# Kernel optimization log

Hardware: AMD Instinct MI355X
Metric: run time of the kernel (lower is better)

Reference implementation:

```python
import jax, jax.numpy as jnp
import numpy as np
import math

B, T, E = 2, 2048, 1024
D = 1024          # total inner dim (config.head_dim)
H = 16            # n_head
HD = D // H       # per-head dim = 64


def setup_inputs() -> dict:
    key = jax.random.key(0)
    k1, k2, k3, k4, k5 = jax.random.split(key, 5)
    s = 0.02
    return {
        "x": jax.random.normal(k1, (B, T, E), dtype=jnp.float32),
        "W_attn": jax.random.normal(k2, (E, 3 * D), dtype=jnp.float32) * s,
        "b_attn": jnp.zeros((3 * D,), dtype=jnp.float32),
        "W_proj": jax.random.normal(k3, (D, E), dtype=jnp.float32) * s,
        "b_proj": jnp.zeros((E,), dtype=jnp.float32),
    }


def reference(x, W_attn, b_attn, W_proj, b_proj):
    Bc, Tc, _ = x.shape
    qkv = x @ W_attn + b_attn                       # [B,T,3D]
    q, k, v = jnp.split(qkv, 3, axis=-1)            # each [B,T,D]
    # reshape to heads: [B,H,T,hd]
    q = q.reshape(Bc, Tc, H, HD).transpose(0, 2, 1, 3)
    k = k.reshape(Bc, Tc, H, HD).transpose(0, 2, 1, 3)
    v = v.reshape(Bc, Tc, H, HD).transpose(0, 2, 1, 3)
    scale = 1.0 / math.sqrt(HD)
    att = jnp.einsum("bhqd,bhkd->bhqk", q, k) * scale   # [B,H,T,T]
    causal = jnp.tril(jnp.ones((Tc, Tc), dtype=bool))
    att = jnp.where(causal[None, None], att, -jnp.inf)
    att = jax.nn.softmax(att, axis=-1)
    y = jnp.einsum("bhqk,bhkd->bhqd", att, v)           # [B,H,T,hd]
    y = y.transpose(0, 2, 1, 3).reshape(Bc, Tc, D)      # [B,T,D]
    return y @ W_proj + b_proj                          # [B,T,E]
```

## Files before the change

kernel.cpp:

```cpp
#include <hip/hip_runtime.h>

typedef unsigned short u16;
typedef unsigned char u8;
typedef signed char s8;
typedef unsigned int u32;
typedef short bf16x8 __attribute__((ext_vector_type(8)));
typedef float f32x4 __attribute__((ext_vector_type(4)));
typedef int i32x4 __attribute__((ext_vector_type(4)));

#define SXI 21.1666667f
#define SWI 1058.3333f
#define DEQ 4.4640015e-5f

__device__ __forceinline__ u16 f2bf(float f) {
  union { float f; u32 u; } v; v.f = f;
  u32 r = v.u + 0x7fffu + ((v.u >> 16) & 1u);
  return (u16)(r >> 16);
}
__device__ __forceinline__ u16 f2bf_fast(float f) {
  union { float f; u32 u; } v; v.f = f;
  return (u16)((v.u + 0x8000u) >> 16);
}
__device__ __forceinline__ s8 q8(float v, float s) {
  float x = fminf(127.f, fmaxf(-127.f, v * s));
  return (s8)__float2int_rn(x);
}
__device__ __forceinline__ float fexp2(float x) {
#if __has_builtin(__builtin_amdgcn_exp2f)
  return __builtin_amdgcn_exp2f(x);
#else
  return exp2f(x);
#endif
}

__device__ __forceinline__ void gld_lds16(const u16* g, u16* l) {
  __builtin_amdgcn_global_load_lds(
      (__attribute__((address_space(1))) u32*)(g),
      (__attribute__((address_space(3))) u32*)(l), 16, 0, 0);
}
__device__ __forceinline__ void gld_lds16b(const u8* g, u8* l) {
  __builtin_amdgcn_global_load_lds(
      (__attribute__((address_space(1))) u32*)(g),
      (__attribute__((address_space(3))) u32*)(l), 16, 0, 0);
}

__device__ __forceinline__ bf16x8 ldsfrag(const u16* base, int row, int c8) {
  return *(const bf16x8*)(base + row * 64 + ((c8 ^ (row & 7)) << 3));
}
__device__ __forceinline__ int swz4(int r) { return (r & 3) ^ ((r >> 2) & 3); }

template <int CTRL>
__device__ __forceinline__ float dppf(float x) {
  return __int_as_float(__builtin_amdgcn_update_dpp(0, __float_as_int(x), CTRL, 0xf, 0xf, true));
}
__device__ __forceinline__ float red16_max(float x) {
  x = fmaxf(x, dppf<0xB1>(x));
  x = fmaxf(x, dppf<0x4E>(x));
  x = fmaxf(x, dppf<0x141>(x));
  x = fmaxf(x, dppf<0x140>(x));
  return x;
}
__device__ __forceinline__ float red16_sum(float x) {
  x += dppf<0xB1>(x);
  x += dppf<0x4E>(x);
  x += dppf<0x141>(x);
  x += dppf<0x140>(x);
  return x;
}

__global__ __launch_bounds__(256) void k_prep(const float* __restrict__ x, u16* __restrict__ xb,
                                              s8* __restrict__ xq,
                                              const float* __restrict__ Wa, u16* __restrict__ WaT,
                                              s8* __restrict__ wq8,
                                              const float* __restrict__ Wp, u16* __restrict__ WpT) {
  __shared__ float t[64][65];
  const int id = blockIdx.x;
  if (id < 2048) {
    int i = (id * 256 + threadIdx.x) * 8;
    const float4* p = (const float4*)(x + i);
    float4 a = p[0], b = p[1];
    uint4 o;
    o.x = (u32)f2bf(a.x) | ((u32)f2bf(a.y) << 16);
    o.y = (u32)f2bf(a.z) | ((u32)f2bf(a.w) << 16);
    o.z = (u32)f2bf(b.x) | ((u32)f2bf(b.y) << 16);
    o.w = (u32)f2bf(b.z) | ((u32)f2bf(b.w) << 16);
    *(uint4*)(xb + i) = o;
    u32 lo = (u32)(u8)q8(a.x, SXI) | ((u32)(u8)q8(a.y, SXI) << 8) |
             ((u32)(u8)q8(a.z, SXI) << 16) | ((u32)(u8)q8(a.w, SXI) << 24);
    u32 hi = (u32)(u8)q8(b.x, SXI) | ((u32)(u8)q8(b.y, SXI) << 8) |
             ((u32)(u8)q8(b.z, SXI) << 16) | ((u32)(u8)q8(b.w, SXI) << 24);
    uint2 oq; oq.x = lo; oq.y = hi;
    *(uint2*)(xq + i) = oq;
  } else if (id < 2816) {
    int q = id - 2048;
    int bx = q % 48, by = q / 48;
    int c0 = bx * 64, r0 = by * 64;
    int tx = threadIdx.x & 63, ty = threadIdx.x >> 6;
#pragma unroll
    for (int i = ty; i < 64; i += 4) t[i][tx] = Wa[(size_t)(r0 + i) * 3072 + c0 + tx];
    __syncthreads();
#pragma unroll
    for (int i = ty; i < 64; i += 4) {
      int row = c0 + i;
      if (row < 2048)
        wq8[(size_t)row * 1024 + r0 + tx] = q8(t[tx][i], SWI);
      else
        WaT[(size_t)row * 1024 + r0 + tx] = f2bf(t[tx][i]);
    }
  } else {
    int q = id - 2816;
    int bx = q & 15, by = q >> 4;
    int c0 = bx * 64, r0 = by * 64;
    int tx = threadIdx.x & 63, ty = threadIdx.x >> 6;
#pragma unroll
    for (int i = ty; i < 64; i += 4) t[i][tx] = Wp[(size_t)(r0 + i) * 1024 + c0 + tx];
    __syncthreads();
#pragma unroll
    for (int i = ty; i < 64; i += 4)
      WpT[(size_t)(c0 + i) * 1024 + r0 + tx] = f2bf(t[tx][i]);
  }
}

__global__ __launch_bounds__(256) void k_gemm_qkv(const u16* __restrict__ xb,
                                                  const s8* __restrict__ xq,
                                                  const u16* __restrict__ Wt,
                                                  const s8* __restrict__ wq8,
                                                  const float* __restrict__ bias,
                                                  u16* __restrict__ qb, u16* __restrict__ kb,
                                                  u16* __restrict__ vtb) {
  const int id = blockIdx.x;
  const int tid = threadIdx.x;
  const int lane = tid & 63, w = tid >> 6;
  const int lr = lane & 15, lq = lane >> 4;

  if (id < 1024) {
    __shared__ __align__(16) u8 la8[64 * 64], lb8[128 * 64];
    const int wm = (w >> 1) << 5, wn = (w & 1) << 6;
    i32x4 acc[2][4];
#pragma unroll
    for (int mi = 0; mi < 2; ++mi)
#pragma unroll
      for (int ni = 0; ni < 4; ++ni) acc[mi][ni] = (i32x4){0, 0, 0, 0};
    const int m0 = (id >> 4) * 64, n0 = (id & 15) * 128;
    const int srow4 = tid >> 2;
    const int gcol4 = (((tid & 3) ^ swz4(srow4)) << 4);
    const u8* ag = (const u8*)xq + (size_t)(m0 + srow4) * 1024 + gcol4;
    const u8* bg = (const u8*)wq8 + (size_t)(n0 + srow4) * 1024 + gcol4;

    for (int k0 = 0; k0 < 1024; k0 += 64) {
      __syncthreads();
      gld_lds16b(ag + k0, la8 + (w * 16) * 64);
#pragma unroll
      for (int r = 0; r < 2; ++r)
        gld_lds16b(bg + (size_t)r * 64 * 1024 + k0, lb8 + (r * 64 + w * 16) * 64);
      __syncthreads();
      i32x4 a[2], b[4];
#pragma unroll
      for (int mi = 0; mi < 2; ++mi) {
        int m = wm + mi * 16 + lr;
        a[mi] = *(const i32x4*)(la8 + m * 64 + ((lq ^ swz4(m)) << 4));
      }
#pragma unroll
      for (int ni = 0; ni < 4; ++ni) {
        int n = wn + ni * 16 + lr;
        b[ni] = *(const i32x4*)(lb8 + n * 64 + ((lq ^ swz4(n)) << 4));
      }
#pragma unroll
      for (int mi = 0; mi < 2; ++mi)
#pragma unroll
        for (int ni = 0; ni < 4; ++ni)
          acc[mi][ni] = __builtin_amdgcn_mfma_i32_16x16x64_i8(a[mi], b[ni], acc[mi][ni], 0, 0, 0);
    }
#pragma unroll
    for (int mi = 0; mi < 2; ++mi) {
      int gm = m0 + wm + mi * 16 + lq * 4;
#pragma unroll
      for (int ni = 0; ni < 4; ++ni) {
        int gn = n0 + wn + ni * 16 + lr;
        float bv = bias[gn];
        int which = gn >> 10, head = (gn >> 6) & 15, hd = gn & 63;
#pragma unroll
        for (int r = 0; r < 4; ++r) {
          int row = gm + r;
          int b2 = row >> 11, tt = row & 2047;
          float v = (float)acc[mi][ni][r] * DEQ + bv;
          size_t bh = (size_t)(b2 * 16 + head);
          if (which == 0)
            qb[(bh * 2048 + tt) * 64 + hd] = f2bf(v * 0.18033688f);
          else
            kb[(bh * 2048 + tt) * 64 + hd] = f2bf(v);
        }
      }
    }
  } else {
    __shared__ u16 sA[64 * 64], sB[128 * 64];
    const int wm = (w >> 1) << 5, wn = (w & 1) << 6;
    f32x4 acc[2][4];
#pragma unroll
    for (int mi = 0; mi < 2; ++mi)
#pragma unroll
      for (int ni = 0; ni < 4; ++ni) acc[mi][ni] = (f32x4){0.f, 0.f, 0.f, 0.f};
    const int t2 = id - 1024;
    const int m0 = (t2 >> 5) * 64, n0 = (t2 & 31) * 128;
    const int srow = tid >> 3;
    const int gcol = ((tid & 7) ^ (srow & 7)) << 3;
    const u16* ag = Wt + 2048 * 1024 + (size_t)(m0 + srow) * 1024 + gcol;
    const u16* bg = xb + (size_t)(n0 + srow) * 1024 + gcol;
    u16* la = sA + w * 512;
    u16* lb = sB + w * 512;

    for (int k0 = 0; k0 < 1024; k0 += 64) {
      __syncthreads();
#pragma unroll
      for (int r = 0; r < 2; ++r) gld_lds16(ag + (size_t)r * 32 * 1024 + k0, la + r * 2048);
#pragma unroll
      for (int r = 0; r < 4; ++r) gld_lds16(bg + (size_t)r * 32 * 1024 + k0, lb + r * 2048);
      __syncthreads();
#pragma unroll
      for (int kk = 0; kk < 64; kk += 32) {
        const int c8 = (kk >> 3) + lq;
        bf16x8 af[2], bfr[4];
#pragma unroll
        for (int i = 0; i < 2; ++i) af[i] = ldsfrag(sA, wm + i * 16 + lr, c8);
#pragma unroll
        for (int i = 0; i < 4; ++i) bfr[i] = ldsfrag(sB, wn + i * 16 + lr, c8);
#pragma unroll
        for (int mi = 0; mi < 2; ++mi)
#pragma unroll
          for (int ni = 0; ni < 4; ++ni)
            acc[mi][ni] = __builtin_amdgcn_mfma_f32_16x16x32_bf16(af[mi], bfr[ni], acc[mi][ni], 0, 0, 0);
      }
    }
#pragma unroll
    for (int mi = 0; mi < 2; ++mi) {
      int gm = m0 + wm + mi * 16 + lq * 4;
      float4 bv = *(const float4*)(bias + 2048 + gm);
#pragma unroll
      for (int ni = 0; ni < 4; ++ni) {
        int gn = n0 + wn + ni * 16 + lr;
        int b = gn >> 11, tt = gn & 2047;
#pragma unroll
        for (int r = 0; r < 4; ++r) {
          int dv = gm + r;
          float v = acc[mi][ni][r] + ((const float*)&bv)[r];
          vtb[((size_t)(b * 1024 + dv)) * 2048 + tt] = f2bf(v);
        }
      }
    }
  }
}

__global__ __launch_bounds__(256, 4) void k_attn(const u16* __restrict__ qb,
                                                 const u16* __restrict__ kb,
                                                 const u16* __restrict__ vtb,
                                                 u16* __restrict__ yb) {
  __shared__ u16 sK[2][64 * 64];
  __shared__ u16 sV[2][64 * 64];
  __shared__ u16 sP[64 * 64];

  const int tid = threadIdx.x;
  const int lane = tid & 63, w = tid >> 6;
  const int lr = lane & 15, lq = lane >> 4;
  const int l = blockIdx.x;
  const int bh = l & 31;
  const int i = l >> 5;
  int qt;
  if (i < 8) qt = 31 - i;
  else if (i < 16) qt = i - 8;
  else if (i < 24) qt = 39 - i;
  else qt = i - 16;
  const int q0 = qt << 6;
  const int NT = qt + 1;

  const u16* qh = qb + (size_t)bh * (2048 * 64);
  const u16* kh = kb + (size_t)bh * (2048 * 64);
  const u16* vh = vtb + (size_t)bh * (64 * 2048);

  bf16x8 qreg[2];
  {
    const u16* qp = qh + (size_t)(q0 + w * 16 + lr) * 64 + lq * 8;
    qreg[0] = *(const bf16x8*)(qp);
    qreg[1] = *(const bf16x8*)(qp + 32);
  }

  const int srow = tid >> 3;
  const int gcol = ((tid & 7) ^ (srow & 7)) << 3;

  u16* pP[4][4];
#pragma unroll
  for (int nj = 0; nj < 4; ++nj) {
    int chunk = nj * 2 + (lr >> 3);
#pragma unroll
    for (int r = 0; r < 4; ++r) {
      int row = w * 16 + lq * 4 + r;
      pP[nj][r] = sP + row * 64 + ((chunk ^ (row & 7)) << 3) + (lr & 7);
    }
  }

  {
    u16* lk0 = sK[0] + w * 512;
    u16* lv0 = sV[0] + w * 512;
#pragma unroll
    for (int r = 0; r < 2; ++r) {
      gld_lds16(kh + (size_t)(r * 32 + srow) * 64 + gcol, lk0 + r * 2048);
      gld_lds16(vh + (size_t)(r * 32 + srow) * 2048 + gcol, lv0 + r * 2048);
    }
    if (NT > 1) {
      u16* lk1 = sK[1] + w * 512;
#pragma unroll
      for (int r = 0; r < 2; ++r)
        gld_lds16(kh + (size_t)(64 + r * 32 + srow) * 64 + gcol, lk1 + r * 2048);
    }
  }
  __syncthreads();

  f32x4 s[4];
#pragma unroll
  for (int nj = 0; nj < 4; ++nj) s[nj] = (f32x4){0.f, 0.f, 0.f, 0.f};
#pragma unroll
  for (int kk = 0; kk < 64; kk += 32) {
    const int c8 = (kk >> 3) + lq;
    bf16x8 kf[4];
#pragma unroll
    for (int nj = 0; nj < 4; ++nj) kf[nj] = ldsfrag(sK[0], nj * 16 + lr, c8);
#pragma unroll
    for (int nj = 0; nj < 4; ++nj)
      s[nj] = __builtin_amdgcn_mfma_f32_16x16x32_bf16(qreg[kk >> 5], kf[nj], s[nj], 0, 0, 0);
  }

  f32x4 o[4];
  float mL2[4], lrp[4];
#pragma unroll
  for (int j = 0; j < 4; ++j) {
    o[j] = (f32x4){0.f, 0.f, 0.f, 0.f};
    mL2[j] = -1e30f;
    lrp[j] = 0.f;
  }

  for (int t = 0; t < NT; ++t) {
    __syncthreads();

    if (t + 2 < NT) {
      const int kv = (t + 2) << 6;
      u16* lk = sK[t & 1] + w * 512;
#pragma unroll
      for (int r = 0; r < 2; ++r)
        gld_lds16(kh + (size_t)(kv + r * 32 + srow) * 64 + gcol, lk + r * 2048);
    }
    if (t + 1 < NT) {
      const int kv = (t + 1) << 6;
      u16* lv = sV[(t + 1) & 1] + w * 512;
#pragma unroll
      for (int r = 0; r < 2; ++r)
        gld_lds16(vh + (size_t)(r * 32 + srow) * 2048 + kv + gcol, lv + r * 2048);
    }

    f32x4 sn[4];
    if (t + 1 < NT) {
      const u16* nK = sK[(t + 1) & 1];
#pragma unroll
      for (int nj = 0; nj < 4; ++nj) sn[nj] = (f32x4){0.f, 0.f, 0.f, 0.f};
#pragma unroll
      for (int kk = 0; kk < 64; kk += 32) {
        const int c8 = (kk >> 3) + lq;
        bf16x8 kf[4];
#pragma unroll
        for (int nj = 0; nj < 4; ++nj) kf[nj] = ldsfrag(nK, nj * 16 + lr, c8);
#pragma unroll
        for (int nj = 0; nj < 4; ++nj)
          sn[nj] = __builtin_amdgcn_mfma_f32_16x16x32_bf16(qreg[kk >> 5], kf[nj], sn[nj], 0, 0, 0);
      }
    }

    if (t == qt) {
      int rloc = w * 16 + lq * 4;
#pragma unroll
      for (int nj = 0; nj < 4; ++nj) {
        int cloc = nj * 16 + lr;
#pragma unroll
        for (int r = 0; r < 4; ++r)
          if (cloc > rloc + r) s[nj][r] = -1e30f;
      }
    }

    float mx[4];
#pragma unroll
    for (int r = 0; r < 4; ++r)
      mx[r] = red16_max(fmaxf(fmaxf(s[0][r], s[1][r]), fmaxf(s[2][r], s[3][r])));
    int need = 0;
#pragma unroll
    for (int r = 0; r < 4; ++r) need |= (mx[r] > mL2[r] + 8.f) ? 1 : 0;
    if (__any(need)) {
#pragma unroll
      for (int r = 0; r < 4; ++r) {
        float mn = fmaxf(mL2[r], mx[r]);
        float al = fexp2(mL2[r] - mn);
        mL2[r] = mn;
        lrp[r] *= al;
#pragma unroll
        for (int nj = 0; nj < 4; ++nj) o[nj][r] *= al;
      }
    }
#pragma unroll
    for (int nj = 0; nj < 4; ++nj)
#pragma unroll
      for (int r = 0; r < 4; ++r) {
        float pp = fexp2(s[nj][r] - mL2[r]);
        s[nj][r] = pp;
        lrp[r] += pp;
      }

#pragma unroll
    for (int nj = 0; nj < 4; ++nj)
#pragma unroll
      for (int r = 0; r < 4; ++r) *pP[nj][r] = f2bf_fast(s[nj][r]);
    asm volatile("s_waitcnt lgkmcnt(0)" ::: "memory");

    {
      const u16* cV = sV[t & 1];
#pragma unroll
      for (int kk = 0; kk < 64; kk += 32) {
        const int c8 = (kk >> 3) + lq;
        bf16x8 pa = ldsfrag(sP, w * 16 + lr, c8);
        bf16x8 vf[4];
#pragma unroll
        for (int nj = 0; nj < 4; ++nj) vf[nj] = ldsfrag(cV, nj * 16 + lr, c8);
#pragma unroll
        for (int nj = 0; nj < 4; ++nj)
          o[nj] = __builtin_amdgcn_mfma_f32_16x16x32_bf16(pa, vf[nj], o[nj], 0, 0, 0);
      }
    }

    if (t + 1 < NT) {
#pragma unroll
      for (int nj = 0; nj < 4; ++nj) s[nj] = sn[nj];
    }
  }

  const int b = bh >> 4, h = bh & 15;
#pragma unroll
  for (int r = 0; r < 4; ++r) {
    float inv = 1.0f / red16_sum(lrp[r]);
    int row = q0 + w * 16 + lq * 4 + r;
    size_t base = ((size_t)(b * 2048 + row)) * 1024 + h * 64;
#pragma unroll
    for (int nj = 0; nj < 4; ++nj) yb[base + nj * 16 + lr] = f2bf(o[nj][r] * inv);
  }
}

__global__ __launch_bounds__(256) void k_gemm_proj(const u16* __restrict__ ybuf,
                                                   const u16* __restrict__ Wt,
                                                   const float* __restrict__ bias,
                                                   float* __restrict__ out) {
  __shared__ u16 sA[64 * 64], sB[64 * 64];
  f32x4 acc[2][2];
#pragma unroll
  for (int mi = 0; mi < 2; ++mi)
#pragma unroll
    for (int ni = 0; ni < 2; ++ni) acc[mi][ni] = (f32x4){0.f, 0.f, 0.f, 0.f};

  const int m0 = blockIdx.y * 64, n0 = blockIdx.x * 64;
  const int tid = threadIdx.x;
  const int lane = tid & 63, w = tid >> 6;
  const int wm = (w >> 1) << 5, wn = (w & 1) << 5;
  const int lr = lane & 15, lq = lane >> 4;
  const int srow = tid >> 3;
  const int gcol = ((tid & 7) ^ (srow & 7)) << 3;
  const u16* ag = ybuf + (size_t)(m0 + srow) * 1024 + gcol;
  const u16* bg = Wt + (size_t)(n0 + srow) * 1024 + gcol;
  u16* la = sA + w * 512;
  u16* lb = sB + w * 512;

  for (int k0 = 0; k0 < 1024; k0 += 64) {
    __syncthreads();
#pragma unroll
    for (int r = 0; r < 2; ++r) {
      gld_lds16(ag + (size_t)r * 32 * 1024 + k0, la + r * 2048);
      gld_lds16(bg + (size_t)r * 32 * 1024 + k0, lb + r * 2048);
    }
    __syncthreads();
#pragma unroll
    for (int kk = 0; kk < 64; kk += 32) {
      const int c8 = (kk >> 3) + lq;
      bf16x8 af[2], bfr[2];
#pragma unroll
      for (int i = 0; i < 2; ++i) {
        af[i] = ldsfrag(sA, wm + i * 16 + lr, c8);
        bfr[i] = ldsfrag(sB, wn + i * 16 + lr, c8);
      }
#pragma unroll
      for (int mi = 0; mi < 2; ++mi)
#pragma unroll
        for (int ni = 0; ni < 2; ++ni)
          acc[mi][ni] = __builtin_amdgcn_mfma_f32_16x16x32_bf16(af[mi], bfr[ni], acc[mi][ni], 0, 0, 0);
    }
  }

#pragma unroll
  for (int mi = 0; mi < 2; ++mi) {
    int gm = m0 + wm + mi * 16 + lq * 4;
#pragma unroll
    for (int ni = 0; ni < 2; ++ni) {
      int gn = n0 + wn + ni * 16 + lr;
      float bv = bias[gn];
#pragma unroll
      for (int r = 0; r < 4; ++r) out[(size_t)(gm + r) * 1024 + gn] = acc[mi][ni][r] + bv;
    }
  }
}

extern "C" void kernel_launch(void* const* d_in, const int* in_sizes, int n_in,
                              void* d_out, int out_size, void* d_ws, size_t ws_size,
                              hipStream_t stream) {
  const float* x = (const float*)d_in[0];
  const float* W_attn = (const float*)d_in[1];
  const float* b_attn = (const float*)d_in[2];
  const float* W_proj = (const float*)d_in[3];
  const float* b_proj = (const float*)d_in[4];
  float* out = (float*)d_out;

  u16* ws = (u16*)d_ws;
  u16* xb = ws;
  u16* WaT = ws + 4194304;
  u16* WpT = ws + 7340032;
  u16* qbuf = ws + 8388608;
  u16* kbuf = ws + 12582912;
  u16* vtb = ws + 16777216;
  u16* ybuf = ws + 20971520;
  s8* xq = (s8*)ybuf;
  s8* wq8 = (s8*)ybuf + 4194304;

  k_prep<<<dim3(3072), dim3(256), 0, stream>>>(x, xb, xq, W_attn, WaT, wq8, W_proj, WpT);
  k_gemm_qkv<<<dim3(1536), dim3(256), 0, stream>>>(xb, xq, WaT, wq8, b_attn, qbuf, kbuf, vtb);
  k_attn<<<dim3(1024), dim3(256), 0, stream>>>(qbuf, kbuf, vtb, ybuf);
  k_gemm_proj<<<dim3(16, 64), dim3(256), 0, stream>>>(ybuf, WpT, b_proj, out);
}
```

Baseline: 173.7 us.

## Balance causal attention blocks by pairing q-tiles and splitting KV with merge kernel

```diff
diff --git a/kernel.cpp b/kernel.cpp
--- a/kernel.cpp
+++ b/kernel.cpp
@@ -250,10 +250,12 @@
   }
 }
 
-__global__ __launch_bounds__(256, 4) void k_attn(const u16* __restrict__ qb,
-                                                 const u16* __restrict__ kb,
-                                                 const u16* __restrict__ vtb,
-                                                 u16* __restrict__ yb) {
+__global__ __launch_bounds__(256, 4) void k_attn(const u16* __restrict__ qbp,
+                                                 const u16* __restrict__ kbp,
+                                                 const u16* __restrict__ vtp,
+                                                 u16* __restrict__ yb,
+                                                 float* __restrict__ po,
+                                                 float* __restrict__ pml) {
   __shared__ u16 sK[2][64 * 64];
   __shared__ u16 sV[2][64 * 64];
   __shared__ u16 sP[64 * 64];
@@ -263,24 +265,30 @@
   const int lr = lane & 15, lq = lane >> 4;
   const int l = blockIdx.x;
   const int bh = l & 31;
-  const int i = l >> 5;
-  int qt;
-  if (i < 8) qt = 31 - i;
-  else if (i < 16) qt = i - 8;
-  else if (i < 24) qt = 39 - i;
-  else qt = i - 16;
-  const int q0 = qt << 6;
-  const int NT = qt + 1;
-
-  const u16* qh = qb + (size_t)bh * (2048 * 64);
-  const u16* kh = kb + (size_t)bh * (2048 * 64);
-  const u16* vh = vtb + (size_t)bh * (64 * 2048);
-
-  bf16x8 qreg[2];
+  const int u = l >> 5;
+  const bool isX = (u < 16);
+  const int p = isX ? u : (u - 16);
+  const int NT = isX ? 17 : 16;
+  const int pSw = isX ? p : -1;
+  const int maskT = isX ? p : 15;
+  const int kvY = 16 - p;
+
+  const u16* qh = qbp + (size_t)bh * (2048 * 64);
+  const u16* kh = kbp + (size_t)bh * (2048 * 64);
+  const u16* vh = vtp + (size_t)bh * (64 * 2048);
+
+  bf16x8 qa0, qa1, qb0, qb1;
   {
-    const u16* qp = qh + (size_t)(q0 + w * 16 + lr) * 64 + lq * 8;
-    qreg[0] = *(const bf16x8*)(qp);
-    qreg[1] = *(const bf16x8*)(qp + 32);
+    const u16* qpb = qh + (size_t)(((31 - p) << 6) + w * 16 + lr) * 64 + lq * 8;
+    qb0 = *(const bf16x8*)(qpb);
+    qb1 = *(const bf16x8*)(qpb + 32);
+    if (isX) {
+      const u16* qpa = qh + (size_t)((p << 6) + w * 16 + lr) * 64 + lq * 8;
+      qa0 = *(const bf16x8*)(qpa);
+      qa1 = *(const bf16x8*)(qpa + 32);
+    } else {
+      qa0 = qb0; qa1 = qb1;
+    }
   }
 
   const int srow = tid >> 3;
@@ -298,18 +306,16 @@
   }
 
   {
+    const int kv0 = isX ? 0 : kvY;
+    const int kv1 = isX ? ((1 <= p) ? 1 : 0) : (kvY + 1);
     u16* lk0 = sK[0] + w * 512;
+    u16* lk1 = sK[1] + w * 512;
     u16* lv0 = sV[0] + w * 512;
 #pragma unroll
     for (int r = 0; r < 2; ++r) {
-      gld_lds16(kh + (size_t)(r * 32 + srow) * 64 + gcol, lk0 + r * 2048);
-      gld_lds16(vh + (size_t)(r * 32 + srow) * 2048 + gcol, lv0 + r * 2048);
-    }
-    if (NT > 1) {
-      u16* lk1 = sK[1] + w * 512;
-#pragma unroll
-      for (int r = 0; r < 2; ++r)
-        gld_lds16(kh + (size_t)(64 + r * 32 + srow) * 64 + gcol, lk1 + r * 2048);
+      gld_lds16(kh + (size_t)(kv0 * 64 + r * 32 + srow) * 64 + gcol, lk0 + r * 2048);
+      gld_lds16(vh + (size_t)(r * 32 + srow) * 2048 + kv0 * 64 + gcol, lv0 + r * 2048);
+      gld_lds16(kh + (size_t)(kv1 * 64 + r * 32 + srow) * 64 + gcol, lk1 + r * 2048);
     }
   }
   __syncthreads();
@@ -317,15 +323,19 @@
   f32x4 s[4];
 #pragma unroll
   for (int nj = 0; nj < 4; ++nj) s[nj] = (f32x4){0.f, 0.f, 0.f, 0.f};
-#pragma unroll
-  for (int kk = 0; kk < 64; kk += 32) {
-    const int c8 = (kk >> 3) + lq;
-    bf16x8 kf[4];
-#pragma unroll
-    for (int nj = 0; nj < 4; ++nj) kf[nj] = ldsfrag(sK[0], nj * 16 + lr, c8);
-#pragma unroll
-    for (int nj = 0; nj < 4; ++nj)
-      s[nj] = __builtin_amdgcn_mfma_f32_16x16x32_bf16(qreg[kk >> 5], kf[nj], s[nj], 0, 0, 0);
+  {
+    bf16x8 q0 = (0 <= pSw) ? qa0 : qb0;
+    bf16x8 q1 = (0 <= pSw) ? qa1 : qb1;
+#pragma unroll
+    for (int kk = 0; kk < 64; kk += 32) {
+      const int c8 = (kk >> 3) + lq;
+      bf16x8 kf[4];
+#pragma unroll
+      for (int nj = 0; nj < 4; ++nj) kf[nj] = ldsfrag(sK[0], nj * 16 + lr, c8);
+#pragma unroll
+      for (int nj = 0; nj < 4; ++nj)
+        s[nj] = __builtin_amdgcn_mfma_f32_16x16x32_bf16(kk ? q1 : q0, kf[nj], s[nj], 0, 0, 0);
+    }
   }
 
   f32x4 o[4];
@@ -337,27 +347,33 @@
     lrp[j] = 0.f;
   }
 
+  const int b = bh >> 4, h = bh & 15;
+
   for (int t = 0; t < NT; ++t) {
     __syncthreads();
 
     if (t + 2 < NT) {
-      const int kv = (t + 2) << 6;
+      int j = t + 2;
+      int kv = isX ? ((j <= p) ? j : j - p - 1) : (kvY + j);
       u16* lk = sK[t & 1] + w * 512;
 #pragma unroll
       for (int r = 0; r < 2; ++r)
-        gld_lds16(kh + (size_t)(kv + r * 32 + srow) * 64 + gcol, lk + r * 2048);
+        gld_lds16(kh + (size_t)(kv * 64 + r * 32 + srow) * 64 + gcol, lk + r * 2048);
     }
     if (t + 1 < NT) {
-      const int kv = (t + 1) << 6;
+      int j = t + 1;
+      int kv = isX ? ((j <= p) ? j : j - p - 1) : (kvY + j);
       u16* lv = sV[(t + 1) & 1] + w * 512;
 #pragma unroll
       for (int r = 0; r < 2; ++r)
-        gld_lds16(vh + (size_t)(r * 32 + srow) * 2048 + kv + gcol, lv + r * 2048);
+        gld_lds16(vh + (size_t)(r * 32 + srow) * 2048 + kv * 64 + gcol, lv + r * 2048);
     }
 
     f32x4 sn[4];
     if (t + 1 < NT) {
       const u16* nK = sK[(t + 1) & 1];
+      bf16x8 q0 = (t + 1 <= pSw) ? qa0 : qb0;
+      bf16x8 q1 = (t + 1 <= pSw) ? qa1 : qb1;
 #pragma unroll
       for (int nj = 0; nj < 4; ++nj) sn[nj] = (f32x4){0.f, 0.f, 0.f, 0.f};
 #pragma unroll
@@ -368,11 +384,11 @@
         for (int nj = 0; nj < 4; ++nj) kf[nj] = ldsfrag(nK, nj * 16 + lr, c8);
 #pragma unroll
         for (int nj = 0; nj < 4; ++nj)
-          sn[nj] = __builtin_amdgcn_mfma_f32_16x16x32_bf16(qreg[kk >> 5], kf[nj], sn[nj], 0, 0, 0);
-      }
-    }
-
-    if (t == qt) {
+          sn[nj] = __builtin_amdgcn_mfma_f32_16x16x32_bf16(kk ? q1 : q0, kf[nj], sn[nj], 0, 0, 0);
+      }
+    }
+
+    if (t == maskT) {
       int rloc = w * 16 + lq * 4;
 #pragma unroll
       for (int nj = 0; nj < 4; ++nj) {
@@ -431,20 +447,70 @@
       }
     }
 
+    if (isX && t == p) {
+#pragma unroll
+      for (int r = 0; r < 4; ++r) {
+        float inv = 1.0f / red16_sum(lrp[r]);
+        int row = (p << 6) + w * 16 + lq * 4 + r;
+        size_t base = ((size_t)(b * 2048 + row)) * 1024 + h * 64;
+#pragma unroll
+        for (int nj = 0; nj < 4; ++nj) yb[base + nj * 16 + lr] = f2bf(o[nj][r] * inv);
+      }
+#pragma unroll
+      for (int j = 0; j < 4; ++j) {
+        o[j] = (f32x4){0.f, 0.f, 0.f, 0.f};
+        mL2[j] = -1e30f;
+        lrp[j] = 0.f;
+      }
+    }
+
     if (t + 1 < NT) {
 #pragma unroll
       for (int nj = 0; nj < 4; ++nj) s[nj] = sn[nj];
     }
   }
 
+  {
+    const int pi = bh * 16 + p;
+    const int S = isX ? 0 : 1;
+    float* poo = po + (size_t)(pi * 2 + S) * 4096;
+    float* pmm = pml + (size_t)(pi * 2 + S) * 128;
+#pragma unroll
+    for (int r = 0; r < 4; ++r) {
+      float ls = red16_sum(lrp[r]);
+      int row = w * 16 + lq * 4 + r;
+      if (lr == 0) {
+        pmm[row * 2] = mL2[r];
+        pmm[row * 2 + 1] = ls;
+      }
+#pragma unroll
+      for (int nj = 0; nj < 4; ++nj) poo[row * 64 + nj * 16 + lr] = o[nj][r];
+    }
+  }
+}
+
+__global__ __launch_bounds__(256) void k_merge(const float* __restrict__ po,
+                                               const float* __restrict__ pml,
+                                               u16* __restrict__ yb) {
+  const int pi = blockIdx.x;
+  const int bh = pi >> 4, p = pi & 15;
   const int b = bh >> 4, h = bh & 15;
-#pragma unroll
-  for (int r = 0; r < 4; ++r) {
-    float inv = 1.0f / red16_sum(lrp[r]);
-    int row = q0 + w * 16 + lq * 4 + r;
-    size_t base = ((size_t)(b * 2048 + row)) * 1024 + h * 64;
-#pragma unroll
-    for (int nj = 0; nj < 4; ++nj) yb[base + nj * 16 + lr] = f2bf(o[nj][r] * inv);
+  const int q0 = (31 - p) << 6;
+  const float* oX = po + (size_t)(pi * 2 + 0) * 4096;
+  const float* oY = po + (size_t)(pi * 2 + 1) * 4096;
+  const float* mlX = pml + (size_t)(pi * 2 + 0) * 128;
+  const float* mlY = pml + (size_t)(pi * 2 + 1) * 128;
+#pragma unroll
+  for (int k = 0; k < 16; ++k) {
+    int idx = k * 256 + threadIdx.x;
+    int row = idx >> 6, col = idx & 63;
+    float mX = mlX[row * 2], lX = mlX[row * 2 + 1];
+    float mY = mlY[row * 2], lY = mlY[row * 2 + 1];
+    float m = fmaxf(mX, mY);
+    float aX = fexp2(mX - m), aY = fexp2(mY - m);
+    float linv = 1.0f / (lX * aX + lY * aY);
+    float y = (oX[idx] * aX + oY[idx] * aY) * linv;
+    yb[((size_t)(b * 2048 + q0 + row)) * 1024 + h * 64 + col] = f2bf(y);
   }
 }
 
@@ -522,16 +588,19 @@
   u16* ws = (u16*)d_ws;
   u16* xb = ws;
   u16* WaT = ws + 4194304;
-  u16* WpT = ws + 7340032;
   u16* qbuf = ws + 8388608;
   u16* kbuf = ws + 12582912;
   u16* vtb = ws + 16777216;
   u16* ybuf = ws + 20971520;
   s8* xq = (s8*)ybuf;
   s8* wq8 = (s8*)ybuf + 4194304;
+  float* po = (float*)ws;
+  float* pml = (float*)(ws + 25165824);
+  u16* WpT = ws + 25427968;
 
   k_prep<<<dim3(3072), dim3(256), 0, stream>>>(x, xb, xq, W_attn, WaT, wq8, W_proj, WpT);
   k_gemm_qkv<<<dim3(1536), dim3(256), 0, stream>>>(xb, xq, WaT, wq8, b_attn, qbuf, kbuf, vtb);
-  k_attn<<<dim3(1024), dim3(256), 0, stream>>>(qbuf, kbuf, vtb, ybuf);
+  k_attn<<<dim3(1024), dim3(256), 0, stream>>>(qbuf, kbuf, vtb, ybuf, po, pml);
+  k_merge<<<dim3(512), dim3(256), 0, stream>>>(po, pml, ybuf);
   k_gemm_proj<<<dim3(16, 64), dim3(256), 0, stream>>>(ybuf, WpT, b_proj, out);
 }
```

Measured after the change: 175.2 us. About the same (+0.8%).
